# Performance work log

Measured on AMD Instinct MI355X. Metric: run time of the kernel, lower is better.

Reference implementation:

```python
import jax, jax.numpy as jnp
import numpy as np

A = 9  # len(scales) * len(ratios) anchor templates
DN = ('NHWC', 'HWIO', 'NHWC')


def _conv(x, w, b):
    y = jax.lax.conv_general_dilated(x, w, window_strides=(1, 1), padding='SAME',
                                     dimension_numbers=DN)
    return y + b


def setup_inputs() -> dict:
    key = jax.random.key(0)
    ks = jax.random.split(key, 9)
    s = 0.02  # weight init scale
    x = jax.random.normal(ks[0], (4, 128, 128, 512), jnp.float32)
    W1 = jax.random.normal(ks[1], (3, 3, 512, 256), jnp.float32) * s
    b1 = jnp.zeros((256,), jnp.float32)
    W2 = jax.random.normal(ks[2], (3, 3, 256, 256), jnp.float32) * s
    b2 = jnp.zeros((256,), jnp.float32)
    Wr = jax.random.normal(ks[3], (1, 1, 256, 4 * A), jnp.float32) * s
    br = jnp.zeros((4 * A,), jnp.float32)
    Wc = jax.random.normal(ks[4], (1, 1, 256, 2 * A), jnp.float32) * s
    bc = jnp.zeros((2 * A,), jnp.float32)
    return {'x': x, 'W1': W1, 'b1': b1, 'W2': W2, 'b2': b2,
            'Wr': Wr, 'br': br, 'Wc': Wc, 'bc': bc}


def reference(x, W1, b1, W2, b2, Wr, br, Wc, bc):
    h = jax.nn.relu(_conv(x, W1, b1))
    h = jax.nn.relu(_conv(h, W2, b2))
    B, H, W = h.shape[0], h.shape[1], h.shape[2]
    reg = _conv(h, Wr, br).reshape(B, H, W, A, 4)            # (B,H,W,A,4)
    cls = _conv(h, Wc, bc).reshape(B, H, W, A, 2)            # (B,H,W,A,2)
    cls = jax.nn.softmax(cls, axis=4)
    return jnp.concatenate((cls, reg), axis=4)               # (B,H,W,A,6)
```

## Files before the change

kernel.cpp:

```cpp
#include <hip/hip_runtime.h>


typedef float f32x4  __attribute__((ext_vector_type(4)));
typedef float f32x16 __attribute__((ext_vector_type(16)));
typedef short bf16x8 __attribute__((ext_vector_type(8)));

union U16x8 { uint4 v; unsigned short s[8]; };

__device__ __forceinline__ unsigned short f2bf(float f) {
  union { float f; unsigned int u; } v; v.f = f;
  unsigned int r = v.u + 0x7FFFu + ((v.u >> 16) & 1u);
  return (unsigned short)(r >> 16);
}

#define GLOAD_LDS16(G, L)                                        \
  __builtin_amdgcn_global_load_lds(                              \
      (const __attribute__((address_space(1))) void*)(G),        \
      (__attribute__((address_space(3))) void*)(L), 16, 0, 0)

__global__ __launch_bounds__(256) void transpose_cvt(
    const float* __restrict__ src, unsigned short* __restrict__ dst,
    int K, int N) {
  __shared__ float t[32][33];
  const int tx = threadIdx.x, ty = threadIdx.y;
  const int k0 = blockIdx.x * 32, n0 = blockIdx.y * 32;
  const float* s = src + (size_t)blockIdx.z * K * N;
  unsigned short* d = dst + (size_t)blockIdx.z * N * K;
#pragma unroll
  for (int r = 0; r < 32; r += 8) {
    int k = k0 + ty + r, n = n0 + tx;
    t[ty + r][tx] = (k < K && n < N) ? s[(size_t)k * N + n] : 0.f;
  }
  __syncthreads();
#pragma unroll
  for (int r = 0; r < 32; r += 8) {
    int n = n0 + ty + r, k = k0 + tx;
    if (n < N && k < K) d[(size_t)n * K + k] = f2bf(t[tx][ty + r]);
  }
}

__global__ __launch_bounds__(256) void pack_w(
    const float* __restrict__ W, unsigned short* __restrict__ out, int CIN) {
  const int NCI = CIN / 32;
  int tid = blockIdx.x * 256 + threadIdx.x;
  int co = tid & 255;
  int q  = (tid >> 8) & 3;
  int t  = tid >> 10;
  int dx = t % 3;
  int r  = t / 3;
  int kt = r % NCI;
  int dy = r / NCI;
  U16x8 u;
#pragma unroll
  for (int e = 0; e < 8; ++e) {
    int ci = kt * 32 + q * 8 + e;
    u.s[e] = f2bf(W[((size_t)(dy * 3 + dx) * CIN + ci) * 256 + co]);
  }
  *(uint4*)(out + (size_t)tid * 8) = u.v;
}

__global__ __launch_bounds__(256) void convert_x(
    const float* __restrict__ x, unsigned short* __restrict__ xp) {
  int idx = blockIdx.x * 256 + threadIdx.x;
  int g = idx & 63;
  int cell = idx >> 6;
  int xpix = cell % 130;
  int t = cell / 130;
  int ypix = t % 130;
  int b = t / 130;
  U16x8 u;
  if (xpix == 0 || xpix == 129 || ypix == 0 || ypix == 129) {
    u.v = make_uint4(0u, 0u, 0u, 0u);
  } else {
    const float* sp = x + ((size_t)((b * 128 + ypix - 1) * 128) + (xpix - 1)) * 512 + g * 8;
    float4 a = *(const float4*)sp;
    float4 c = *(const float4*)(sp + 4);
    u.s[0] = f2bf(a.x); u.s[1] = f2bf(a.y); u.s[2] = f2bf(a.z); u.s[3] = f2bf(a.w);
    u.s[4] = f2bf(c.x); u.s[5] = f2bf(c.y); u.s[6] = f2bf(c.z); u.s[7] = f2bf(c.w);
  }
  *(uint4*)(xp + (((size_t)(b * 130 + ypix) * 64 + g) * 130 + xpix) * 8) = u.v;
}

__global__ __launch_bounds__(256) void zero_h1_borders(unsigned short* __restrict__ h1p) {
  int idx = blockIdx.x * 256 + threadIdx.x;
  int px = idx % 130;
  int t = idx / 130;
  int g = t & 31;
  int tt = t >> 5;
  int y = tt % 130;
  int b = tt / 130;
  if (px == 0 || px == 129 || y == 0 || y == 129)
    *(uint4*)(h1p + (((size_t)(b * 130 + y) * 32 + g) * 130 + px) * 8) =
        make_uint4(0u, 0u, 0u, 0u);
}

template<int CIN, int MODE>
__global__ __launch_bounds__(512, 2) void conv3x3(
    const unsigned short* __restrict__ Ap,
    const unsigned short* __restrict__ WTp,
    const float* __restrict__ bias,
    unsigned short* __restrict__ out) {
  constexpr int NCI    = CIN / 32;
  constexpr int LOGNCI = (NCI == 16) ? 4 : 3;
  constexpr int NT     = 3 * NCI;
  constexpr int GPR    = CIN / 8;
  constexpr int PXS    = 136;
  constexpr int A_BYTES = 8 * PXS * 16;
  constexpr int B_BYTES = 12 * 256 * 16;
  constexpr int BUF     = A_BYTES + B_BYTES;
  __shared__ __align__(16) unsigned char smem[2 * BUF];

  const int tid  = threadIdx.x;
  const int wave = tid >> 6, lane = tid & 63;
  const int l31 = lane & 31, hi = lane >> 5;
  const int wm = wave >> 2, wn = wave & 3;
  const int b = blockIdx.x >> 6;
  const int y0 = (blockIdx.x & 63) * 2;
  const int brow = b * 130 + y0;

  int a_rel[3], a_c[3];
#pragma unroll
  for (int i = 0; i < 3; ++i) {
    int s = wave + i * 8;
    if (s < 17) {
      int c = s * 64 + lane;
      int px = c % PXS, t2 = c / PXS;
      int q = t2 & 3, rw = t2 >> 2;
      a_rel[i] = (rw * GPR + q) * 1040 + px * 8;
      a_c[i] = c * 16;
    } else { a_rel[i] = 0; a_c[i] = 0; }
  }

  const float bb0 = bias[wn * 64 + l31];
  const float bb1 = bias[wn * 64 + 32 + l31];

  f32x16 acc[4][2] = {};

  auto stage = [&](int tile) {
    const int dy = tile >> LOGNCI;
    const int kt = tile & (NCI - 1);
    unsigned char* sb = smem + (size_t)(tile & 1) * BUF;
    const unsigned short* Ab = Ap + ((size_t)(brow + dy) * GPR + kt * 4) * 1040;
    GLOAD_LDS16(Ab + a_rel[0], sb + a_c[0]);
    GLOAD_LDS16(Ab + a_rel[1], sb + a_c[1]);
    if (wave == 0) GLOAD_LDS16(Ab + a_rel[2], sb + a_c[2]);
    const unsigned short* Bb = WTp + (size_t)(dy * NCI + kt) * 24576;
#pragma unroll
    for (int i = 0; i < 6; ++i) {
      int c = (wave * 6 + i) * 64 + lane;
      GLOAD_LDS16(Bb + (size_t)c * 8, sb + A_BYTES + c * 16);
    }
  };

  stage(0);
  asm volatile("s_waitcnt vmcnt(0)" ::: "memory");
  __builtin_amdgcn_s_barrier();

#pragma unroll 2
  for (int t = 0; t < NT; ++t) {
    const unsigned char* sb = smem + (size_t)(t & 1) * BUF;
#pragma unroll
    for (int dx = 0; dx < 3; ++dx) {
      bf16x8 af[2][4], bfr[2][2];
#pragma unroll
      for (int ks = 0; ks < 2; ++ks) {
        const int q_ = ks * 2 + hi;
        const int ab = ((wm * 4 + q_) * PXS + dx + l31) * 16;
        const int bb = A_BYTES + ((dx * 4 + q_) * 256 + wn * 64 + l31) * 16;
#pragma unroll
        for (int i = 0; i < 4; ++i)
          af[ks][i] = *(const bf16x8*)(sb + ab + i * 512);
#pragma unroll
        for (int j = 0; j < 2; ++j)
          bfr[ks][j] = *(const bf16x8*)(sb + bb + j * 512);
      }
      if (dx == 0 && t + 1 < NT) stage(t + 1);
      if (dx == 2 && t + 1 < NT)
        asm volatile("s_waitcnt vmcnt(0)" ::: "memory");
      __builtin_amdgcn_sched_barrier(0);
      __builtin_amdgcn_s_barrier();
      asm volatile("s_waitcnt lgkmcnt(0)" ::: "memory");
      __builtin_amdgcn_sched_barrier(0);
      __builtin_amdgcn_s_setprio(1);
#pragma unroll
      for (int ks = 0; ks < 2; ++ks)
#pragma unroll
        for (int i = 0; i < 4; ++i)
#pragma unroll
          for (int j = 0; j < 2; ++j)
            acc[i][j] = __builtin_amdgcn_mfma_f32_32x32x16_bf16(
                af[ks][i], bfr[ks][j], acc[i][j], 0, 0, 0);
      __builtin_amdgcn_s_setprio(0);
      __builtin_amdgcn_sched_barrier(0);
      __builtin_amdgcn_s_barrier();
    }
  }

#pragma unroll
  for (int i = 0; i < 4; ++i) {
#pragma unroll
    for (int j = 0; j < 2; ++j) {
      const int n = wn * 64 + j * 32 + l31;
      const float bb = j ? bb1 : bb0;
#pragma unroll
      for (int reg = 0; reg < 16; ++reg) {
        int px = i * 32 + (reg & 3) + 8 * (reg >> 2) + 4 * hi;
        float v = fmaxf(acc[i][j][reg] + bb, 0.f);
        size_t off;
        if (MODE == 0)
          off = (((size_t)(brow + wm + 1) * 32 + (n >> 3)) * 130 + (px + 1)) * 8 + (n & 7);
        else
          off = ((size_t)((b * 128 + y0 + wm) * 128) + px) * 256 + n;
        out[off] = f2bf(v);
      }
    }
  }
}

__global__ __launch_bounds__(256) void heads_kernel(
    const unsigned short* __restrict__ h2,
    const unsigned short* __restrict__ WhT,
    const float* __restrict__ br, const float* __restrict__ bc,
    float* __restrict__ out) {
  __shared__ __align__(16) unsigned short As[64][264];
  const int tid = threadIdx.x;
  const int wave = tid >> 6, lane = tid & 63;
  const int quad = lane >> 4, l16 = lane & 15;
  const int pix0 = blockIdx.x * 64;
#pragma unroll
  for (int r = 0; r < 8; ++r) {
    int s = r * 256 + tid;
    int row = s >> 5, seg = s & 31;
    *(uint4*)&As[row][seg * 8] =
        *(const uint4*)(h2 + (size_t)(pix0 + row) * 256 + seg * 8);
  }
  __syncthreads();
  f32x4 acc[4] = {};
#pragma unroll
  for (int ks = 0; ks < 8; ++ks) {
    bf16x8 af = *(const bf16x8*)&As[wave * 16 + l16][ks * 32 + quad * 8];
#pragma unroll
    for (int j = 0; j < 4; ++j) {
      bf16x8 bfr = *(const bf16x8*)(WhT + (size_t)(j * 16 + l16) * 256 + ks * 32 + quad * 8);
      acc[j] = __builtin_amdgcn_mfma_f32_16x16x32_bf16(af, bfr, acc[j], 0, 0, 0);
    }
  }
#pragma unroll
  for (int j = 0; j < 4; ++j) {
    int n = j * 16 + l16;
    float bias = 0.f;
    if (n < 18) bias = bc[n];
    else if (n < 54) bias = br[n - 18];
#pragma unroll
    for (int r = 0; r < 4; ++r) {
      int p = pix0 + wave * 16 + quad * 4 + r;
      float v = acc[j][r] + bias;
      float partner = __shfl_xor(v, 1);
      if (n < 18) {
        float mx = fmaxf(v, partner);
        float e0 = __expf(v - mx), e1 = __expf(partner - mx);
        int a = n >> 1, sl = n & 1;
        out[(size_t)p * 54 + a * 6 + sl] = e0 / (e0 + e1);
      } else if (n < 54) {
        int rr = n - 18, a = rr >> 2, sl = (rr & 3) + 2;
        out[(size_t)p * 54 + a * 6 + sl] = v;
      }
    }
  }
}

extern "C" void kernel_launch(void* const* d_in, const int* in_sizes, int n_in,
                              void* d_out, int out_size, void* d_ws, size_t ws_size,
                              hipStream_t stream) {
  const float* x  = (const float*)d_in[0];
  const float* W1 = (const float*)d_in[1];
  const float* b1 = (const float*)d_in[2];
  const float* W2 = (const float*)d_in[3];
  const float* b2 = (const float*)d_in[4];
  const float* Wr = (const float*)d_in[5];
  const float* br = (const float*)d_in[6];
  const float* Wc = (const float*)d_in[7];
  const float* bc = (const float*)d_in[8];
  float* out = (float*)d_out;

  constexpr size_t XPAD_B  = 4ull * 130 * 130 * 512 * 2;
  constexpr size_t H1PAD_B = 4ull * 130 * 130 * 256 * 2;
  constexpr size_t H2_B    = 4ull * 128 * 128 * 256 * 2;
  constexpr size_t W1T_B   = 9ull * 256 * 512 * 2;
  constexpr size_t W2T_B   = 9ull * 256 * 256 * 2;
  char* ws = (char*)d_ws;
  unsigned short* x_pad  = (unsigned short*)(ws);
  unsigned short* h1_pad = (unsigned short*)(ws + XPAD_B);
  unsigned short* h2     = (unsigned short*)(ws + XPAD_B + H1PAD_B);
  unsigned short* W1T    = (unsigned short*)(ws + XPAD_B + H1PAD_B + H2_B);
  unsigned short* W2T    = (unsigned short*)(ws + XPAD_B + H1PAD_B + H2_B + W1T_B);
  unsigned short* WhT    = (unsigned short*)(ws + XPAD_B + H1PAD_B + H2_B + W1T_B + W2T_B);

  hipMemsetAsync(WhT, 0, 64ull * 256 * 2, stream);
  pack_w<<<576, 256, 0, stream>>>(W1, W1T, 512);
  pack_w<<<288, 256, 0, stream>>>(W2, W2T, 256);
  transpose_cvt<<<dim3(8, 1, 1),  dim3(32, 8), 0, stream>>>(Wc, WhT, 256, 18);
  transpose_cvt<<<dim3(8, 2, 1),  dim3(32, 8), 0, stream>>>(Wr, WhT + 18 * 256, 256, 36);
  convert_x<<<16900, 256, 0, stream>>>(x, x_pad);
  zero_h1_borders<<<8450, 256, 0, stream>>>(h1_pad);
  conv3x3<512, 0><<<256, 512, 0, stream>>>(x_pad, W1T, b1, h1_pad);
  conv3x3<256, 1><<<256, 512, 0, stream>>>(h1_pad, W2T, b2, h2);
  heads_kernel<<<1024, 256, 0, stream>>>(h2, WhT, br, bc, out);
}
```

Measured before the change: 462.0 us.

## Split LDS fragment loads to overlap MFMA and retile input conversion via LDS

The conv inner loop now loads the two k-slices of A/B fragments in separate groups and waits only for the first group (lgkmcnt(6)) before issuing its MFMAs, so the second group's LDS reads overlap the first half of the math. The input conversion kernel is rewritten to stage a 32-pixel row segment through swizzled shared memory, so both the global reads and the channel-group-major writes to the padded layout are coalesced. Border zeroing is generalised and run as a separate kernel for both padded buffers, which adds a launch that scans the whole padded x layout. The partial lgkmcnt wait assumes the compiler issues the LDS reads in source order.

```diff
diff --git a/kernel.cpp b/kernel.cpp
--- a/kernel.cpp
+++ b/kernel.cpp
@@ -59,38 +59,52 @@
   *(uint4*)(out + (size_t)tid * 8) = u.v;
 }
 
-__global__ __launch_bounds__(256) void convert_x(
+__global__ __launch_bounds__(256) void convert_x_t(
     const float* __restrict__ x, unsigned short* __restrict__ xp) {
-  int idx = blockIdx.x * 256 + threadIdx.x;
-  int g = idx & 63;
-  int cell = idx >> 6;
-  int xpix = cell % 130;
-  int t = cell / 130;
-  int ypix = t % 130;
-  int b = t / 130;
-  U16x8 u;
-  if (xpix == 0 || xpix == 129 || ypix == 0 || ypix == 129) {
-    u.v = make_uint4(0u, 0u, 0u, 0u);
-  } else {
-    const float* sp = x + ((size_t)((b * 128 + ypix - 1) * 128) + (xpix - 1)) * 512 + g * 8;
-    float4 a = *(const float4*)sp;
-    float4 c = *(const float4*)(sp + 4);
-    u.s[0] = f2bf(a.x); u.s[1] = f2bf(a.y); u.s[2] = f2bf(a.z); u.s[3] = f2bf(a.w);
-    u.s[4] = f2bf(c.x); u.s[5] = f2bf(c.y); u.s[6] = f2bf(c.z); u.s[7] = f2bf(c.w);
-  }
-  *(uint4*)(xp + (((size_t)(b * 130 + ypix) * 64 + g) * 130 + xpix) * 8) = u.v;
-}
-
-__global__ __launch_bounds__(256) void zero_h1_borders(unsigned short* __restrict__ h1p) {
+  __shared__ __align__(16) unsigned short t[32 * 64 * 8];
+  const int tid = threadIdx.x;
+  const int blk = blockIdx.x;
+  const int pxb = blk & 3;
+  const int y   = (blk >> 2) & 127;
+  const int b   = blk >> 9;
+  const int px0 = pxb * 32 + 1;
+  {
+    const int g = tid & 63, pl = tid >> 6;
+#pragma unroll
+    for (int it = 0; it < 8; ++it) {
+      int pxl = it * 4 + pl;
+      const float* sp = x + ((size_t)((b * 128 + y) * 128) + (px0 - 1 + pxl)) * 512 + g * 8;
+      float4 a = *(const float4*)sp;
+      float4 c = *(const float4*)(sp + 4);
+      U16x8 u;
+      u.s[0] = f2bf(a.x); u.s[1] = f2bf(a.y); u.s[2] = f2bf(a.z); u.s[3] = f2bf(a.w);
+      u.s[4] = f2bf(c.x); u.s[5] = f2bf(c.y); u.s[6] = f2bf(c.z); u.s[7] = f2bf(c.w);
+      *(uint4*)&t[((size_t)pxl * 64 + (g ^ (pxl & 7))) * 8] = u.v;
+    }
+  }
+  __syncthreads();
+  {
+    const int pxl = tid & 31, gh = tid >> 5;
+#pragma unroll
+    for (int it = 0; it < 8; ++it) {
+      int g = it * 8 + gh;
+      uint4 v = *(const uint4*)&t[((size_t)pxl * 64 + (g ^ (pxl & 7))) * 8];
+      *(uint4*)(xp + (((size_t)(b * 130 + y + 1) * 64 + g) * 130 + (px0 + pxl)) * 8) = v;
+    }
+  }
+}
+
+__global__ __launch_bounds__(256) void zero_borders(
+    unsigned short* __restrict__ p, int GPR) {
   int idx = blockIdx.x * 256 + threadIdx.x;
   int px = idx % 130;
   int t = idx / 130;
-  int g = t & 31;
-  int tt = t >> 5;
+  int g = t % GPR;
+  int tt = t / GPR;
   int y = tt % 130;
   int b = tt / 130;
-  if (px == 0 || px == 129 || y == 0 || y == 129)
-    *(uint4*)(h1p + (((size_t)(b * 130 + y) * 32 + g) * 130 + px) * 8) =
+  if (b < 4 && (px == 0 || px == 129 || y == 0 || y == 129))
+    *(uint4*)(p + (((size_t)(b * 130 + y) * GPR + g) * 130 + px) * 8) =
         make_uint4(0u, 0u, 0u, 0u);
 }
 
@@ -162,34 +176,51 @@
 #pragma unroll
     for (int dx = 0; dx < 3; ++dx) {
       bf16x8 af[2][4], bfr[2][2];
-#pragma unroll
-      for (int ks = 0; ks < 2; ++ks) {
-        const int q_ = ks * 2 + hi;
+      {
+        const int q_ = hi;
         const int ab = ((wm * 4 + q_) * PXS + dx + l31) * 16;
         const int bb = A_BYTES + ((dx * 4 + q_) * 256 + wn * 64 + l31) * 16;
 #pragma unroll
         for (int i = 0; i < 4; ++i)
-          af[ks][i] = *(const bf16x8*)(sb + ab + i * 512);
+          af[0][i] = *(const bf16x8*)(sb + ab + i * 512);
 #pragma unroll
         for (int j = 0; j < 2; ++j)
-          bfr[ks][j] = *(const bf16x8*)(sb + bb + j * 512);
+          bfr[0][j] = *(const bf16x8*)(sb + bb + j * 512);
+      }
+      __builtin_amdgcn_sched_barrier(0);
+      {
+        const int q_ = 2 + hi;
+        const int ab = ((wm * 4 + q_) * PXS + dx + l31) * 16;
+        const int bb = A_BYTES + ((dx * 4 + q_) * 256 + wn * 64 + l31) * 16;
+#pragma unroll
+        for (int i = 0; i < 4; ++i)
+          af[1][i] = *(const bf16x8*)(sb + ab + i * 512);
+#pragma unroll
+        for (int j = 0; j < 2; ++j)
+          bfr[1][j] = *(const bf16x8*)(sb + bb + j * 512);
       }
       if (dx == 0 && t + 1 < NT) stage(t + 1);
       if (dx == 2 && t + 1 < NT)
         asm volatile("s_waitcnt vmcnt(0)" ::: "memory");
       __builtin_amdgcn_sched_barrier(0);
       __builtin_amdgcn_s_barrier();
+      asm volatile("s_waitcnt lgkmcnt(6)" ::: "memory");
+      __builtin_amdgcn_sched_barrier(0);
+      __builtin_amdgcn_s_setprio(1);
+#pragma unroll
+      for (int i = 0; i < 4; ++i)
+#pragma unroll
+        for (int j = 0; j < 2; ++j)
+          acc[i][j] = __builtin_amdgcn_mfma_f32_32x32x16_bf16(
+              af[0][i], bfr[0][j], acc[i][j], 0, 0, 0);
       asm volatile("s_waitcnt lgkmcnt(0)" ::: "memory");
       __builtin_amdgcn_sched_barrier(0);
-      __builtin_amdgcn_s_setprio(1);
-#pragma unroll
-      for (int ks = 0; ks < 2; ++ks)
-#pragma unroll
-        for (int i = 0; i < 4; ++i)
-#pragma unroll
-          for (int j = 0; j < 2; ++j)
-            acc[i][j] = __builtin_amdgcn_mfma_f32_32x32x16_bf16(
-                af[ks][i], bfr[ks][j], acc[i][j], 0, 0, 0);
+#pragma unroll
+      for (int i = 0; i < 4; ++i)
+#pragma unroll
+        for (int j = 0; j < 2; ++j)
+          acc[i][j] = __builtin_amdgcn_mfma_f32_32x32x16_bf16(
+              af[1][i], bfr[1][j], acc[i][j], 0, 0, 0);
       __builtin_amdgcn_s_setprio(0);
       __builtin_amdgcn_sched_barrier(0);
       __builtin_amdgcn_s_barrier();
@@ -301,8 +332,9 @@
   pack_w<<<288, 256, 0, stream>>>(W2, W2T, 256);
   transpose_cvt<<<dim3(8, 1, 1),  dim3(32, 8), 0, stream>>>(Wc, WhT, 256, 18);
   transpose_cvt<<<dim3(8, 2, 1),  dim3(32, 8), 0, stream>>>(Wr, WhT + 18 * 256, 256, 36);
-  convert_x<<<16900, 256, 0, stream>>>(x, x_pad);
-  zero_h1_borders<<<8450, 256, 0, stream>>>(h1_pad);
+  convert_x_t<<<2048, 256, 0, stream>>>(x, x_pad);
+  zero_borders<<<16900, 256, 0, stream>>>(x_pad, 64);
+  zero_borders<<<8450, 256, 0, stream>>>(h1_pad, 32);
   conv3x3<512, 0><<<256, 512, 0, stream>>>(x_pad, W1T, b1, h1_pad);
   conv3x3<256, 1><<<256, 512, 0, stream>>>(h1_pad, W2T, b2, h2);
   heads_kernel<<<1024, 256, 0, stream>>>(h2, WhT, br, bc, out);
```

Measured after the change: 472.3 us. 2.2% more time.
